# Optimization experiments

Hardware: AMD Instinct MI355X
Metric: run time of the kernel (lower is better)

The kernel has to match this reference:

```python
import jax, jax.numpy as jnp
import numpy as np

P = 8        # patch size
STRIDE = 4   # reference patch stride
SR = 12      # search radius
SS = 3       # search step -> 9x9 = 81 candidates
K = 16       # group size (3rd dim of 3D transform)
LAM = 2.7    # hard threshold multiplier
TWO_STEP = True


def _dct_mat(n):
    k = np.arange(n)[:, None].astype(np.float64)
    i = np.arange(n)[None, :].astype(np.float64)
    m = np.cos(np.pi * (2 * i + 1) * k / (2 * n)) * np.sqrt(2.0 / n)
    m[0] /= np.sqrt(2.0)
    return jnp.asarray(m, jnp.float32)


def _hadamard(n):
    h = np.array([[1.0]])
    while h.shape[0] < n:
        h = np.kron(h, np.array([[1.0, 1.0], [1.0, -1.0]])) / np.sqrt(2.0)
    return jnp.asarray(h, jnp.float32)

D8 = _dct_mat(P)
H16 = _hadamard(K)


def _extract_patches(img):
    # img (H, W) -> (Hp*Wp, P*P) patches at stride 1
    H, W = img.shape
    Hp, Wp = H - P + 1, W - P + 1
    cols = [img[di:di + Hp, dj:dj + Wp] for di in range(P) for dj in range(P)]
    return jnp.stack(cols, -1).reshape(Hp * Wp, P * P), Hp, Wp


def _block_match(patches, Hp, Wp):
    # returns (N, K) flat patch indices of best-matching groups
    ri = jnp.arange(0, Hp, STRIDE)
    rj = jnp.arange(0, Wp, STRIDE)
    RI, RJ = jnp.meshgrid(ri, rj, indexing='ij')
    RI, RJ = RI.reshape(-1), RJ.reshape(-1)                     # (N,)
    offs = jnp.arange(-SR, SR + 1, SS)
    OI, OJ = jnp.meshgrid(offs, offs, indexing='ij')
    ci = jnp.clip(RI[:, None] + OI.reshape(-1)[None, :], 0, Hp - 1)
    cj = jnp.clip(RJ[:, None] + OJ.reshape(-1)[None, :], 0, Wp - 1)
    cidx = ci * Wp + cj                                         # (N, C)
    cand = patches[cidx]                                        # (N, C, 64)
    ref = patches[RI * Wp + RJ]                                 # (N, 64)
    dist = (jnp.sum(cand * cand, -1)
            - 2.0 * jnp.einsum('nce,ne->nc', cand, ref)
            + jnp.sum(ref * ref, -1)[:, None])
    _, top = jax.lax.top_k(-dist, K)
    return jnp.take_along_axis(cidx, top, axis=1)               # (N, K)


def _fwd3d(groups):
    # (N, K, P*P) -> 3D transform coeffs (N, K, P, P)
    g = groups.reshape(groups.shape[0], K, P, P)
    c = jnp.einsum('ab,nkbc,dc->nkad', D8, g, D8)   # 2D DCT per patch
    return jnp.einsum('gk,nkad->ngad', H16, c)      # 1D Hadamard across group


def _inv3d(coef):
    c = jnp.einsum('gk,ngad->nkad', H16, coef)      # H^T (orthonormal)
    g = jnp.einsum('ab,nkad,dc->nkbc', D8, c, D8)   # inverse 2D DCT
    return g.reshape(coef.shape[0], K, P * P)


def _aggregate(vals, w, gidx, Hp, Wp, H, W):
    # vals (N,K,64) filtered patches, w (N,) group weights, gidx (N,K)
    gi, gj = gidx // Wp, gidx % Wp
    offs = (jnp.arange(P)[:, None] * W + jnp.arange(P)[None, :]).reshape(-1)
    pix = ((gi * W + gj)[..., None] + offs).reshape(-1)         # (N*K*64,)
    wv = jnp.broadcast_to(w[:, None, None], vals.shape)
    num = jnp.zeros(H * W, jnp.float32).at[pix].add((wv * vals).reshape(-1))
    den = jnp.zeros(H * W, jnp.float32).at[pix].add(wv.reshape(-1))
    return (num / jnp.maximum(den, 1e-8)).reshape(H, W)


def _bm3d_channel(img, sigma2):
    H, W = img.shape
    sigma2 = jnp.float32(sigma2)
    sigma = jnp.sqrt(sigma2)
    patches, Hp, Wp = _extract_patches(img)

    # ---- step 1: hard-threshold collaborative filtering ----
    gidx = _block_match(patches, Hp, Wp)
    groups = patches[gidx]                                      # (N,K,64)
    coef = _fwd3d(groups)
    mask = (jnp.abs(coef) > LAM * sigma)
    mask = mask.at[:, 0, 0, 0].set(True)                        # keep DC
    coef_ht = jnp.where(mask, coef, 0.0)
    nnz = jnp.sum(mask.astype(jnp.float32), axis=(1, 2, 3))
    w_ht = 1.0 / (sigma2 * jnp.maximum(nnz, 1.0))
    basic = _aggregate(_inv3d(coef_ht), w_ht, gidx, Hp, Wp, H, W)
    if not TWO_STEP:
        return basic

    # ---- step 2: Wiener filtering using the basic estimate ----
    patches_b, _, _ = _extract_patches(basic)
    gidx2 = _block_match(patches_b, Hp, Wp)
    cb = _fwd3d(patches_b[gidx2])                               # basic coeffs
    cn = _fwd3d(patches[gidx2])                                 # noisy coeffs
    wien = cb * cb / (cb * cb + sigma2)
    coef_w = wien * cn
    w_wie = 1.0 / (sigma2 * jnp.maximum(jnp.sum(wien * wien, axis=(1, 2, 3)), 1e-8))
    return _aggregate(_inv3d(coef_w), w_wie, gidx2, Hp, Wp, H, W)


def setup_inputs() -> dict:
    key = jax.random.key(0)
    im = jax.random.randint(key, (1, 1, 384, 384), 0, 256, dtype=jnp.int32)
    return {"im": im, "variance": 25}


def reference(im, variance):
    # im: (1, 1, H, W) int tensor, values >= 0; variance: scalar noise variance
    outs = [_bm3d_channel(im[0, c].astype(jnp.float32), variance)
            for c in range(im.shape[1])]
    return jnp.stack(outs, 0)[None]                             # (1, C, H, W) float32
```

## Files before the change

kernel.cpp:

```cpp
#include <hip/hip_runtime.h>
#include <math.h>

#define TS 60
#define FINF 3.4e38f

__device__ __forceinline__ int iclip(int v, int hi) {
  return v < 0 ? 0 : (v > hi ? hi : v);
}

constexpr float CA = 0.35355339059327373f;
constexpr float K1 = 0.49039264020161522f;
constexpr float K2 = 0.46193976625564337f;
constexpr float K3 = 0.41573480615127262f;
constexpr float K4 = 0.35355339059327379f;
constexpr float K5 = 0.27778511650980111f;
constexpr float K6 = 0.19134171618254489f;
constexpr float K7 = 0.097545161008064135f;

constexpr float DCT8[8][8] = {
  { CA, CA, CA, CA, CA, CA, CA, CA},
  { K1, K3, K5, K7,-K7,-K5,-K3,-K1},
  { K2, K6,-K6,-K2,-K2,-K6, K6, K2},
  { K3,-K7,-K1,-K5, K5, K1, K7,-K3},
  { K4,-K4,-K4, K4, K4,-K4,-K4, K4},
  { K5,-K1, K7, K3,-K3,-K7, K1,-K5},
  { K6,-K2, K2,-K6,-K6, K2,-K2, K6},
  { K7,-K5, K3,-K1, K1,-K3, K5,-K7},
};

__device__ __forceinline__ int sxor_i(int v, int m) {
  switch (m) {
    case 1:  return __builtin_amdgcn_update_dpp(0, v, 0xB1, 0xF, 0xF, true);
    case 2:  return __builtin_amdgcn_update_dpp(0, v, 0x4E, 0xF, 0xF, true);
    case 4:  return __builtin_amdgcn_ds_swizzle(v, (4 << 10) | 0x1F);
    case 8:  return __builtin_amdgcn_ds_swizzle(v, (8 << 10) | 0x1F);
    case 16: return __builtin_amdgcn_ds_swizzle(v, (16 << 10) | 0x1F);
    default: return __shfl_xor(v, 32, 64);
  }
}
__device__ __forceinline__ float sxor_f(float v, int m) {
  return __int_as_float(sxor_i(__float_as_int(v), m));
}

__device__ __forceinline__ float qbcast(float v, int s) {
  int x = __float_as_int(v), r;
  switch (s) {
    case 0:  r = __builtin_amdgcn_update_dpp(0, x, 0x00, 0xF, 0xF, true); break;
    case 1:  r = __builtin_amdgcn_update_dpp(0, x, 0x55, 0xF, 0xF, true); break;
    case 2:  r = __builtin_amdgcn_update_dpp(0, x, 0xAA, 0xF, 0xF, true); break;
    default: r = __builtin_amdgcn_update_dpp(0, x, 0xFF, 0xF, 0xF, true); break;
  }
  return __int_as_float(r);
}

__device__ __forceinline__ void fwd_rowcol(float X[2][8], float U[2][8],
                                           const float Ca0[8], const float Ca1[8]) {
#pragma unroll
  for (int r = 0; r < 2; r++)
#pragma unroll
    for (int d = 0; d < 8; d++) {
      float s = X[r][0] * DCT8[d][0];
#pragma unroll
      for (int c = 1; c < 8; c++) s += X[r][c] * DCT8[d][c];
      U[r][d] = s;
    }
#pragma unroll
  for (int r = 0; r < 2; r++)
#pragma unroll
    for (int d = 0; d < 8; d++) X[r][d] = 0.f;
#pragma unroll
  for (int b = 0; b < 8; b++)
#pragma unroll
    for (int d = 0; d < 8; d++) {
      float yb = qbcast(U[b & 1][d], b >> 1);
      X[0][d] += Ca0[b] * yb;
      X[1][d] += Ca1[b] * yb;
    }
}

__device__ __forceinline__ void inv_colrow(float X[2][8], float U[2][8],
                                           const float Ct0[8], const float Ct1[8]) {
#pragma unroll
  for (int r = 0; r < 2; r++)
#pragma unroll
    for (int d = 0; d < 8; d++) U[r][d] = 0.f;
#pragma unroll
  for (int a = 0; a < 8; a++)
#pragma unroll
    for (int d = 0; d < 8; d++) {
      float za = qbcast(X[a & 1][d], a >> 1);
      U[0][d] += Ct0[a] * za;
      U[1][d] += Ct1[a] * za;
    }
#pragma unroll
  for (int r = 0; r < 2; r++)
#pragma unroll
    for (int c = 0; c < 8; c++) {
      float s = U[r][0] * DCT8[0][c];
#pragma unroll
      for (int d = 1; d < 8; d++) s += U[r][d] * DCT8[d][c];
      X[r][c] = s;
    }
}

__device__ __forceinline__ void had16r(float X[2][8], int lane) {
#pragma unroll
  for (int m = 4; m <= 32; m <<= 1) {
    bool hi = (lane & m) != 0;
#pragma unroll
    for (int r = 0; r < 2; r++)
#pragma unroll
      for (int d = 0; d < 8; d++) {
        float tv = sxor_f(X[r][d], m);
        X[r][d] = hi ? (tv - X[r][d]) : (X[r][d] + tv);
      }
  }
#pragma unroll
  for (int r = 0; r < 2; r++)
#pragma unroll
    for (int d = 0; d < 8; d++) X[r][d] *= 0.25f;
}

template <int WIEN>
__global__ __launch_bounds__(512, 2) void bm3d_pass(
    const int* __restrict__ img, const float* __restrict__ basic,
    const int* __restrict__ pvar,
    float* __restrict__ num, float* __restrict__ den) {
  __shared__ float ldsD[64];
  __shared__ float wdist[8][81];
  __shared__ int   wsel[8][16];
  __shared__ float bufA[32 * TS];
  __shared__ float bufB[32 * TS];

  int t = threadIdx.x;
  int brow = blockIdx.x / 12, bcb = blockIdx.x - brow * 12;
  int ri = brow * 4;
  int bim = ri - 12;       int bi = bim < 0 ? 0 : (bim > 352 ? 352 : bim);
  int ubm = 32 * bcb - 12; int ub = ubm < 0 ? 0 : (ubm > 324 ? 324 : ubm);

  if (t < 64) ldsD[t] = DCT8[t >> 3][t & 7];

  if (t < 480) {
    int r = t / 15, c4 = (t - r * 15) << 2;
    int gidx = (bi + r) * 384 + ub + c4;
    int o = r * TS + c4;
    int4 iv = *(const int4*)&img[gidx];
    float4 fv = make_float4((float)iv.x, (float)iv.y, (float)iv.z, (float)iv.w);
    if (WIEN) {
      *(float4*)&bufA[o] = *(const float4*)&basic[gidx];
      *(float4*)&bufB[o] = fv;
    } else {
      *(float4*)&bufA[o] = fv;
    }
  }
  __syncthreads();

  float sigma2 = (float)pvar[0];
  int wv = t >> 6, lane = t & 63;
  int gc = bcb * 8 + wv;
  bool active = gc < 95;
  int gcw = active ? gc : 94;
  int rj = gcw * 4;

  const float* tileS = bufA;
  const float* tileN = WIEN ? bufB : bufA;

  int cB = lane < 17 ? 64 + lane : 80;
  int ai0 = iclip(ri + (lane / 9) * 3 - 12, 376) - bi;
  int aj0 = iclip(rj + (lane % 9) * 3 - 12, 376) - ub;
  int ai1 = iclip(ri + (cB / 9) * 3 - 12, 376) - bi;
  int aj1 = iclip(rj + (cB % 9) * 3 - 12, 376) - ub;
  int roi = ri - bi, roj = rj - ub;
  float scc0 = 0.f, scr0 = 0.f, scc1 = 0.f, scr1 = 0.f, srr = 0.f;
#pragma unroll
  for (int i = 0; i < 8; i++) {
    const float* rr = tileS + (roi + i) * TS + roj;
    const float* ar = tileS + (ai0 + i) * TS + aj0;
    const float* br = tileS + (ai1 + i) * TS + aj1;
#pragma unroll
    for (int j = 0; j < 8; j++) {
      float rv = rr[j], av = ar[j], bv = br[j];
      scc0 += av * av; scr0 += av * rv;
      scc1 += bv * bv; scr1 += bv * rv;
      srr  += rv * rv;
    }
  }
  float d0 = scc0 - 2.f * scr0 + srr;
  float d1 = lane < 17 ? (scc1 - 2.f * scr1 + srr) : FINF;

  wdist[wv][lane] = d0;
  if (lane < 17) wdist[wv][64 + lane] = d1;
  __syncthreads();

  int rank0 = 0, rank1 = 0;
#pragma unroll 3
  for (int c2 = 0; c2 < 81; c2++) {
    float dd = wdist[wv][c2];
    rank0 += (dd < d0) || (dd == d0 && c2 < lane) ? 1 : 0;
    rank1 += (dd < d1) || (dd == d1 && c2 < 64 + lane) ? 1 : 0;
  }
  if (rank0 < 16) wsel[wv][rank0] = (ai0 << 8) | aj0;
  if (lane < 17 && rank1 < 16) wsel[wv][rank1] = (ai1 << 8) | aj1;
  __syncthreads();

  int k = lane >> 2, q = lane & 3;
  int sp = wsel[wv][k];
  int gi0 = (sp >> 8) + 2 * q, gj0 = sp & 255;

  float Ca0[8], Ca1[8];
#pragma unroll
  for (int b = 0; b < 8; b++) {
    Ca0[b] = ldsD[(2 * q) * 8 + b];
    Ca1[b] = ldsD[(2 * q + 1) * 8 + b];
  }

  float X[2][8], U[2][8], ZB[2][8];
  float w;

  if (WIEN) {
#pragma unroll
    for (int r = 0; r < 2; r++)
#pragma unroll
      for (int c = 0; c < 8; c++) ZB[r][c] = tileS[(gi0 + r) * TS + gj0 + c];
    fwd_rowcol(ZB, U, Ca0, Ca1);
    had16r(ZB, lane);
  }

#pragma unroll
  for (int r = 0; r < 2; r++)
#pragma unroll
    for (int c = 0; c < 8; c++) X[r][c] = tileN[(gi0 + r) * TS + gj0 + c];
  fwd_rowcol(X, U, Ca0, Ca1);
  had16r(X, lane);

  if (WIEN) {
    float part = 0.f;
#pragma unroll
    for (int r = 0; r < 2; r++)
#pragma unroll
      for (int d = 0; d < 8; d++) {
        float cb = ZB[r][d];
        float we = cb * cb / (cb * cb + sigma2);
        X[r][d] = we * X[r][d];
        part += we * we;
      }
#pragma unroll
    for (int m = 1; m <= 32; m <<= 1) part += sxor_f(part, m);
    w = 1.f / (sigma2 * fmaxf(part, 1e-8f));
  } else {
    float thr = 2.7f * sqrtf(sigma2);
    int cnt = 0;
#pragma unroll
    for (int r = 0; r < 2; r++)
#pragma unroll
      for (int d = 0; d < 8; d++) {
        bool keep = (fabsf(X[r][d]) > thr) || (lane == 0 && r == 0 && d == 0);
        cnt += (int)__popcll(__ballot(keep));
        if (!keep) X[r][d] = 0.f;
      }
    w = 1.f / (sigma2 * fmaxf((float)cnt, 1.f));
  }

  had16r(X, lane);
#pragma unroll
  for (int a = 0; a < 8; a++) {
    Ca0[a] = ldsD[a * 8 + 2 * q];
    Ca1[a] = ldsD[a * 8 + 2 * q + 1];
  }
  inv_colrow(X, U, Ca0, Ca1);

  __syncthreads();
  for (int e = t; e < 32 * TS; e += 512) { bufA[e] = 0.f; bufB[e] = 0.f; }
  __syncthreads();

  if (active) {
#pragma unroll
    for (int r = 0; r < 2; r++)
#pragma unroll
      for (int c = 0; c < 8; c++) {
        int off = (gi0 + r) * TS + gj0 + c;
        atomicAdd(&bufA[off], w * X[r][c]);
        atomicAdd(&bufB[off], w);
      }
  }
  __syncthreads();

  for (int e = t; e < 32 * TS; e += 512) {
    float dv = bufB[e];
    if (dv != 0.f) {
      int r = e / TS, c = e - r * TS;
      int gp = (bi + r) * 384 + ub + c;
      atomicAdd(&num[gp], bufA[e]);
      atomicAdd(&den[gp], dv);
    }
  }
}

__global__ void div_kernel(const float* __restrict__ num,
                           const float* __restrict__ den,
                           float* __restrict__ out, int npix) {
  int i = blockIdx.x * blockDim.x + threadIdx.x;
  if (i < npix) out[i] = num[i] / fmaxf(den[i], 1e-8f);
}

extern "C" void kernel_launch(void* const* d_in, const int* in_sizes, int n_in,
                              void* d_out, int out_size, void* d_ws, size_t ws_size,
                              hipStream_t stream) {
  const int* img  = (const int*)d_in[0];
  const int* pvar = (const int*)d_in[1];
  float* out = (float*)d_out;
  float* ws  = (float*)d_ws;

  const int NPIX = 384 * 384;
  float* num1  = ws + 0 * NPIX;
  float* den1  = ws + 1 * NPIX;
  float* basic = ws + 2 * NPIX;
  float* num2  = ws + 3 * NPIX;
  float* den2  = ws + 4 * NPIX;

  hipMemsetAsync(num1, 0, (size_t)2 * NPIX * sizeof(float), stream);
  hipMemsetAsync(num2, 0, (size_t)2 * NPIX * sizeof(float), stream);

  const int NBLK = 95 * 12;
  bm3d_pass<0><<<NBLK, 512, 0, stream>>>(img, nullptr, pvar, num1, den1);
  div_kernel<<<(NPIX + 255) / 256, 256, 0, stream>>>(num1, den1, basic, NPIX);
  bm3d_pass<1><<<NBLK, 512, 0, stream>>>(img, basic, pvar, num2, den2);
  div_kernel<<<(NPIX + 255) / 256, 256, 0, stream>>>(num2, den2, out, NPIX);
}
```

Measured before the change: 324.6 us.

## Process two reference groups per wavefront and halve block size

Each 64-lane wavefront now handles two neighbouring reference patches instead of one. Block matching, ranking, the forward and inverse 3D transforms and aggregation are all interleaved across both groups, and the Hadamard shuffles are fused. Block size drops from 512 to 256 threads with launch bounds raised to four blocks per SM. The block-level barriers between distance write, rank and selection are removed, since each wave only reads its own rows. It also adds a transposed DCT table in LDS and float4 LDS reads for the distance ranking, aiming for more ILP and fewer redundant reference loads, at the cost of higher register pressure.

```diff
diff --git a/kernel.cpp b/kernel.cpp
--- a/kernel.cpp
+++ b/kernel.cpp
@@ -103,7 +103,7 @@
     }
 }
 
-__device__ __forceinline__ void had16r(float X[2][8], int lane) {
+__device__ __forceinline__ void had16r2(float X0[2][8], float X1[2][8], int lane) {
 #pragma unroll
   for (int m = 4; m <= 32; m <<= 1) {
     bool hi = (lane & m) != 0;
@@ -111,24 +111,26 @@
     for (int r = 0; r < 2; r++)
 #pragma unroll
       for (int d = 0; d < 8; d++) {
-        float tv = sxor_f(X[r][d], m);
-        X[r][d] = hi ? (tv - X[r][d]) : (X[r][d] + tv);
-      }
-  }
-#pragma unroll
-  for (int r = 0; r < 2; r++)
-#pragma unroll
-    for (int d = 0; d < 8; d++) X[r][d] *= 0.25f;
+        float t0 = sxor_f(X0[r][d], m);
+        float t1 = sxor_f(X1[r][d], m);
+        X0[r][d] = hi ? (t0 - X0[r][d]) : (X0[r][d] + t0);
+        X1[r][d] = hi ? (t1 - X1[r][d]) : (X1[r][d] + t1);
+      }
+  }
+#pragma unroll
+  for (int r = 0; r < 2; r++)
+#pragma unroll
+    for (int d = 0; d < 8; d++) { X0[r][d] *= 0.25f; X1[r][d] *= 0.25f; }
 }
 
 template <int WIEN>
-__global__ __launch_bounds__(512, 2) void bm3d_pass(
+__global__ __launch_bounds__(256, 4) void bm3d_pass(
     const int* __restrict__ img, const float* __restrict__ basic,
     const int* __restrict__ pvar,
     float* __restrict__ num, float* __restrict__ den) {
-  __shared__ float ldsD[64];
-  __shared__ float wdist[8][81];
-  __shared__ int   wsel[8][16];
+  __shared__ float ldsD[64], ldsDT[64];
+  __shared__ __align__(16) float wdist[8][84];
+  __shared__ int wsel[8][16];
   __shared__ float bufA[32 * TS];
   __shared__ float bufB[32 * TS];
 
@@ -139,9 +141,10 @@
   int ubm = 32 * bcb - 12; int ub = ubm < 0 ? 0 : (ubm > 324 ? 324 : ubm);
 
   if (t < 64) ldsD[t] = DCT8[t >> 3][t & 7];
-
-  if (t < 480) {
-    int r = t / 15, c4 = (t - r * 15) << 2;
+  else if (t < 128) { int u = t - 64; ldsDT[u] = DCT8[u & 7][u >> 3]; }
+
+  for (int e4 = t; e4 < 480; e4 += 256) {
+    int r = e4 / 15, c4 = (e4 - r * 15) << 2;
     int gidx = (bi + r) * 384 + ub + c4;
     int o = r * TS + c4;
     int4 iv = *(const int4*)&img[gidx];
@@ -157,135 +160,201 @@
 
   float sigma2 = (float)pvar[0];
   int wv = t >> 6, lane = t & 63;
-  int gc = bcb * 8 + wv;
-  bool active = gc < 95;
-  int gcw = active ? gc : 94;
-  int rj = gcw * 4;
+  int s0 = 2 * wv, s1 = 2 * wv + 1;
+  int g0 = bcb * 8 + 2 * wv, g1 = g0 + 1;
+  bool active0 = g0 < 95, active1 = g1 < 95;
+  int rj0 = (active0 ? g0 : 94) * 4;
+  int rj1 = (active1 ? g1 : 94) * 4;
 
   const float* tileS = bufA;
   const float* tileN = WIEN ? bufB : bufA;
 
   int cB = lane < 17 ? 64 + lane : 80;
-  int ai0 = iclip(ri + (lane / 9) * 3 - 12, 376) - bi;
-  int aj0 = iclip(rj + (lane % 9) * 3 - 12, 376) - ub;
-  int ai1 = iclip(ri + (cB / 9) * 3 - 12, 376) - bi;
-  int aj1 = iclip(rj + (cB % 9) * 3 - 12, 376) - ub;
-  int roi = ri - bi, roj = rj - ub;
-  float scc0 = 0.f, scr0 = 0.f, scc1 = 0.f, scr1 = 0.f, srr = 0.f;
+  int oiA = (lane / 9) * 3 - 12, ojA = (lane % 9) * 3 - 12;
+  int oiB = (cB / 9) * 3 - 12,   ojB = (cB % 9) * 3 - 12;
+  int aiA = iclip(ri + oiA, 376) - bi;
+  int aiB = iclip(ri + oiB, 376) - bi;
+  int ajA0 = iclip(rj0 + ojA, 376) - ub, ajA1 = iclip(rj1 + ojA, 376) - ub;
+  int ajB0 = iclip(rj0 + ojB, 376) - ub, ajB1 = iclip(rj1 + ojB, 376) - ub;
+  int roi = ri - bi, roj0 = rj0 - ub, roj1 = rj1 - ub;
+
+  float sA0c = 0.f, sA0r = 0.f, sB0c = 0.f, sB0r = 0.f;
+  float sA1c = 0.f, sA1r = 0.f, sB1c = 0.f, sB1r = 0.f;
+  float srr0 = 0.f, srr1 = 0.f;
 #pragma unroll
   for (int i = 0; i < 8; i++) {
-    const float* rr = tileS + (roi + i) * TS + roj;
-    const float* ar = tileS + (ai0 + i) * TS + aj0;
-    const float* br = tileS + (ai1 + i) * TS + aj1;
+    const float* r0p = tileS + (roi + i) * TS + roj0;
+    const float* r1p = tileS + (roi + i) * TS + roj1;
+    const float* a0p = tileS + (aiA + i) * TS + ajA0;
+    const float* a1p = tileS + (aiA + i) * TS + ajA1;
+    const float* b0p = tileS + (aiB + i) * TS + ajB0;
+    const float* b1p = tileS + (aiB + i) * TS + ajB1;
 #pragma unroll
     for (int j = 0; j < 8; j++) {
-      float rv = rr[j], av = ar[j], bv = br[j];
-      scc0 += av * av; scr0 += av * rv;
-      scc1 += bv * bv; scr1 += bv * rv;
-      srr  += rv * rv;
-    }
-  }
-  float d0 = scc0 - 2.f * scr0 + srr;
-  float d1 = lane < 17 ? (scc1 - 2.f * scr1 + srr) : FINF;
-
-  wdist[wv][lane] = d0;
-  if (lane < 17) wdist[wv][64 + lane] = d1;
+      float rv0 = r0p[j], rv1 = r1p[j];
+      float a0 = a0p[j], a1 = a1p[j], b0 = b0p[j], b1 = b1p[j];
+      sA0c += a0 * a0; sA0r += a0 * rv0;
+      sA1c += a1 * a1; sA1r += a1 * rv1;
+      sB0c += b0 * b0; sB0r += b0 * rv0;
+      sB1c += b1 * b1; sB1r += b1 * rv1;
+      srr0 += rv0 * rv0; srr1 += rv1 * rv1;
+    }
+  }
+  float dA0 = sA0c - 2.f * sA0r + srr0;
+  float dA1 = sA1c - 2.f * sA1r + srr1;
+  float dB0 = lane < 17 ? (sB0c - 2.f * sB0r + srr0) : FINF;
+  float dB1 = lane < 17 ? (sB1c - 2.f * sB1r + srr1) : FINF;
+
+  wdist[s0][lane] = dA0;
+  wdist[s1][lane] = dA1;
+  if (lane < 17)      { wdist[s0][64 + lane] = dB0; wdist[s1][64 + lane] = dB1; }
+  else if (lane < 20) { wdist[s0][64 + lane] = FINF; wdist[s1][64 + lane] = FINF; }
+
+  int rA0 = 0, rB0 = 0, rA1 = 0, rB1 = 0;
+  const float4* wp0 = (const float4*)&wdist[s0][0];
+  const float4* wp1 = (const float4*)&wdist[s1][0];
+  int idxA = lane, idxB = 64 + lane;
+#pragma unroll 3
+  for (int c4 = 0; c4 < 21; c4++) {
+    float4 v0 = wp0[c4], v1 = wp1[c4];
+    float e0[4] = {v0.x, v0.y, v0.z, v0.w};
+    float e1[4] = {v1.x, v1.y, v1.z, v1.w};
+#pragma unroll
+    for (int u = 0; u < 4; u++) {
+      int c2 = c4 * 4 + u;
+      rA0 += (e0[u] < dA0 || (e0[u] == dA0 && c2 < idxA)) ? 1 : 0;
+      rB0 += (e0[u] < dB0 || (e0[u] == dB0 && c2 < idxB)) ? 1 : 0;
+      rA1 += (e1[u] < dA1 || (e1[u] == dA1 && c2 < idxA)) ? 1 : 0;
+      rB1 += (e1[u] < dB1 || (e1[u] == dB1 && c2 < idxB)) ? 1 : 0;
+    }
+  }
+  if (rA0 < 16) wsel[s0][rA0] = (aiA << 8) | ajA0;
+  if (rA1 < 16) wsel[s1][rA1] = (aiA << 8) | ajA1;
+  if (lane < 17) {
+    if (rB0 < 16) wsel[s0][rB0] = (aiB << 8) | ajB0;
+    if (rB1 < 16) wsel[s1][rB1] = (aiB << 8) | ajB1;
+  }
+
+  int k = lane >> 2, q = lane & 3;
+  int sp0 = wsel[s0][k], sp1 = wsel[s1][k];
+  int gi0 = (sp0 >> 8) + 2 * q, gj0 = sp0 & 255;
+  int gi1 = (sp1 >> 8) + 2 * q, gj1 = sp1 & 255;
+
+  float Ca0[8], Ca1[8];
+  *(float4*)&Ca0[0] = *(const float4*)&ldsD[(2 * q) * 8];
+  *(float4*)&Ca0[4] = *(const float4*)&ldsD[(2 * q) * 8 + 4];
+  *(float4*)&Ca1[0] = *(const float4*)&ldsD[(2 * q + 1) * 8];
+  *(float4*)&Ca1[4] = *(const float4*)&ldsD[(2 * q + 1) * 8 + 4];
+
+  float X0[2][8], X1[2][8], U[2][8];
+  float w0, w1;
+
+  if (WIEN) {
+    float Z0[2][8], Z1[2][8];
+#pragma unroll
+    for (int r = 0; r < 2; r++)
+#pragma unroll
+      for (int c = 0; c < 8; c++) {
+        Z0[r][c] = tileS[(gi0 + r) * TS + gj0 + c];
+        Z1[r][c] = tileS[(gi1 + r) * TS + gj1 + c];
+      }
+    fwd_rowcol(Z0, U, Ca0, Ca1);
+    fwd_rowcol(Z1, U, Ca0, Ca1);
+    had16r2(Z0, Z1, lane);
+
+#pragma unroll
+    for (int r = 0; r < 2; r++)
+#pragma unroll
+      for (int c = 0; c < 8; c++) {
+        X0[r][c] = tileN[(gi0 + r) * TS + gj0 + c];
+        X1[r][c] = tileN[(gi1 + r) * TS + gj1 + c];
+      }
+    fwd_rowcol(X0, U, Ca0, Ca1);
+    fwd_rowcol(X1, U, Ca0, Ca1);
+    had16r2(X0, X1, lane);
+
+    float p0 = 0.f, p1 = 0.f;
+#pragma unroll
+    for (int r = 0; r < 2; r++)
+#pragma unroll
+      for (int d = 0; d < 8; d++) {
+        float cb0 = Z0[r][d], cb1 = Z1[r][d];
+        float we0 = cb0 * cb0 / (cb0 * cb0 + sigma2);
+        float we1 = cb1 * cb1 / (cb1 * cb1 + sigma2);
+        X0[r][d] = we0 * X0[r][d];
+        X1[r][d] = we1 * X1[r][d];
+        p0 += we0 * we0; p1 += we1 * we1;
+      }
+#pragma unroll
+    for (int m = 1; m <= 32; m <<= 1) { p0 += sxor_f(p0, m); p1 += sxor_f(p1, m); }
+    w0 = 1.f / (sigma2 * fmaxf(p0, 1e-8f));
+    w1 = 1.f / (sigma2 * fmaxf(p1, 1e-8f));
+  } else {
+#pragma unroll
+    for (int r = 0; r < 2; r++)
+#pragma unroll
+      for (int c = 0; c < 8; c++) {
+        X0[r][c] = tileN[(gi0 + r) * TS + gj0 + c];
+        X1[r][c] = tileN[(gi1 + r) * TS + gj1 + c];
+      }
+    fwd_rowcol(X0, U, Ca0, Ca1);
+    fwd_rowcol(X1, U, Ca0, Ca1);
+    had16r2(X0, X1, lane);
+
+    float thr = 2.7f * sqrtf(sigma2);
+    int cnt0 = 0, cnt1 = 0;
+#pragma unroll
+    for (int r = 0; r < 2; r++)
+#pragma unroll
+      for (int d = 0; d < 8; d++) {
+        bool dc = (lane == 0 && r == 0 && d == 0);
+        bool k0 = (fabsf(X0[r][d]) > thr) || dc;
+        bool k1 = (fabsf(X1[r][d]) > thr) || dc;
+        cnt0 += (int)__popcll(__ballot(k0));
+        cnt1 += (int)__popcll(__ballot(k1));
+        if (!k0) X0[r][d] = 0.f;
+        if (!k1) X1[r][d] = 0.f;
+      }
+    w0 = 1.f / (sigma2 * fmaxf((float)cnt0, 1.f));
+    w1 = 1.f / (sigma2 * fmaxf((float)cnt1, 1.f));
+  }
+
+  had16r2(X0, X1, lane);
+#pragma unroll
+  for (int a = 0; a < 8; a++) {
+    Ca0[a] = ldsDT[(2 * q) * 8 + a];
+    Ca1[a] = ldsDT[(2 * q + 1) * 8 + a];
+  }
+  inv_colrow(X0, U, Ca0, Ca1);
+  inv_colrow(X1, U, Ca0, Ca1);
+
   __syncthreads();
-
-  int rank0 = 0, rank1 = 0;
-#pragma unroll 3
-  for (int c2 = 0; c2 < 81; c2++) {
-    float dd = wdist[wv][c2];
-    rank0 += (dd < d0) || (dd == d0 && c2 < lane) ? 1 : 0;
-    rank1 += (dd < d1) || (dd == d1 && c2 < 64 + lane) ? 1 : 0;
-  }
-  if (rank0 < 16) wsel[wv][rank0] = (ai0 << 8) | aj0;
-  if (lane < 17 && rank1 < 16) wsel[wv][rank1] = (ai1 << 8) | aj1;
+  for (int e = t; e < 32 * TS; e += 256) { bufA[e] = 0.f; bufB[e] = 0.f; }
   __syncthreads();
 
-  int k = lane >> 2, q = lane & 3;
-  int sp = wsel[wv][k];
-  int gi0 = (sp >> 8) + 2 * q, gj0 = sp & 255;
-
-  float Ca0[8], Ca1[8];
-#pragma unroll
-  for (int b = 0; b < 8; b++) {
-    Ca0[b] = ldsD[(2 * q) * 8 + b];
-    Ca1[b] = ldsD[(2 * q + 1) * 8 + b];
-  }
-
-  float X[2][8], U[2][8], ZB[2][8];
-  float w;
-
-  if (WIEN) {
-#pragma unroll
-    for (int r = 0; r < 2; r++)
-#pragma unroll
-      for (int c = 0; c < 8; c++) ZB[r][c] = tileS[(gi0 + r) * TS + gj0 + c];
-    fwd_rowcol(ZB, U, Ca0, Ca1);
-    had16r(ZB, lane);
-  }
-
-#pragma unroll
-  for (int r = 0; r < 2; r++)
-#pragma unroll
-    for (int c = 0; c < 8; c++) X[r][c] = tileN[(gi0 + r) * TS + gj0 + c];
-  fwd_rowcol(X, U, Ca0, Ca1);
-  had16r(X, lane);
-
-  if (WIEN) {
-    float part = 0.f;
-#pragma unroll
-    for (int r = 0; r < 2; r++)
-#pragma unroll
-      for (int d = 0; d < 8; d++) {
-        float cb = ZB[r][d];
-        float we = cb * cb / (cb * cb + sigma2);
-        X[r][d] = we * X[r][d];
-        part += we * we;
-      }
-#pragma unroll
-    for (int m = 1; m <= 32; m <<= 1) part += sxor_f(part, m);
-    w = 1.f / (sigma2 * fmaxf(part, 1e-8f));
-  } else {
-    float thr = 2.7f * sqrtf(sigma2);
-    int cnt = 0;
-#pragma unroll
-    for (int r = 0; r < 2; r++)
-#pragma unroll
-      for (int d = 0; d < 8; d++) {
-        bool keep = (fabsf(X[r][d]) > thr) || (lane == 0 && r == 0 && d == 0);
-        cnt += (int)__popcll(__ballot(keep));
-        if (!keep) X[r][d] = 0.f;
-      }
-    w = 1.f / (sigma2 * fmaxf((float)cnt, 1.f));
-  }
-
-  had16r(X, lane);
-#pragma unroll
-  for (int a = 0; a < 8; a++) {
-    Ca0[a] = ldsD[a * 8 + 2 * q];
-    Ca1[a] = ldsD[a * 8 + 2 * q + 1];
-  }
-  inv_colrow(X, U, Ca0, Ca1);
-
+  if (active0) {
+#pragma unroll
+    for (int r = 0; r < 2; r++)
+#pragma unroll
+      for (int c = 0; c < 8; c++) {
+        int off = (gi0 + r) * TS + gj0 + c;
+        atomicAdd(&bufA[off], w0 * X0[r][c]);
+        atomicAdd(&bufB[off], w0);
+      }
+  }
+  if (active1) {
+#pragma unroll
+    for (int r = 0; r < 2; r++)
+#pragma unroll
+      for (int c = 0; c < 8; c++) {
+        int off = (gi1 + r) * TS + gj1 + c;
+        atomicAdd(&bufA[off], w1 * X1[r][c]);
+        atomicAdd(&bufB[off], w1);
+      }
+  }
   __syncthreads();
-  for (int e = t; e < 32 * TS; e += 512) { bufA[e] = 0.f; bufB[e] = 0.f; }
-  __syncthreads();
-
-  if (active) {
-#pragma unroll
-    for (int r = 0; r < 2; r++)
-#pragma unroll
-      for (int c = 0; c < 8; c++) {
-        int off = (gi0 + r) * TS + gj0 + c;
-        atomicAdd(&bufA[off], w * X[r][c]);
-        atomicAdd(&bufB[off], w);
-      }
-  }
-  __syncthreads();
-
-  for (int e = t; e < 32 * TS; e += 512) {
+
+  for (int e = t; e < 32 * TS; e += 256) {
     float dv = bufB[e];
     if (dv != 0.f) {
       int r = e / TS, c = e - r * TS;
@@ -322,8 +391,8 @@
   hipMemsetAsync(num2, 0, (size_t)2 * NPIX * sizeof(float), stream);
 
   const int NBLK = 95 * 12;
-  bm3d_pass<0><<<NBLK, 512, 0, stream>>>(img, nullptr, pvar, num1, den1);
+  bm3d_pass<0><<<NBLK, 256, 0, stream>>>(img, nullptr, pvar, num1, den1);
   div_kernel<<<(NPIX + 255) / 256, 256, 0, stream>>>(num1, den1, basic, NPIX);
-  bm3d_pass<1><<<NBLK, 512, 0, stream>>>(img, basic, pvar, num2, den2);
+  bm3d_pass<1><<<NBLK, 256, 0, stream>>>(img, basic, pvar, num2, den2);
   div_kernel<<<(NPIX + 255) / 256, 256, 0, stream>>>(num2, den2, out, NPIX);
 }
```

After: 463.5 us. 1.43x slower.
